# Performance work log

Measured on AMD Instinct MI355X. Metric: run time of the kernel, lower is better.

Reference implementation:

```python
import jax
jax.config.update("jax_enable_x64", True)
import jax.numpy as jnp
import numpy as np

B, T, C, H = 4, 4096, 120, 64  # batch, seq, n_embed, head_size


def setup_inputs() -> dict:
    key = jax.random.key(0)
    kx, kk, kq, kv = jax.random.split(key, 4)
    x = jax.random.normal(kx, (B, T, C), dtype=jnp.float32)
    s = 1.0 / np.sqrt(C)  # ~nn.Linear init scale
    Wk = jax.random.normal(kk, (C, H), dtype=jnp.float32) * s
    Wq = jax.random.normal(kq, (C, H), dtype=jnp.float32) * s
    Wv = jax.random.normal(kv, (C, H), dtype=jnp.float32) * s
    return {"x": x, "Wk": Wk, "Wq": Wq, "Wv": Wv}


def reference(x, Wk, Wq, Wv):
    # Original module runs entirely in float64 (.double()).
    x = x.astype(jnp.float64)
    Wk = Wk.astype(jnp.float64)
    Wq = Wq.astype(jnp.float64)
    Wv = Wv.astype(jnp.float64)
    k = jnp.einsum("btc,ch->bth", x, Wk)
    q = jnp.einsum("btc,ch->bth", x, Wq)
    v = jnp.einsum("btc,ch->bth", x, Wv)
    scale = x.shape[-1] ** (-0.5)  # NOTE: scales by n_embed (C), not head_size
    wei = jnp.einsum("bth,bsh->bts", q, k) * scale  # [B, T, T]
    wei = jax.nn.softmax(wei, axis=-1)
    # dropout(p=0.01) is identity in eval mode
    out = jnp.einsum("bts,bsh->bth", wei, v)  # [B, T, H]
    return out
```

## Files before the change

### kernel.cpp

```cpp
#include <hip/hip_runtime.h>

typedef __attribute__((ext_vector_type(2))) float f32x2;
typedef __attribute__((ext_vector_type(4))) float f32x4;
typedef __attribute__((ext_vector_type(8))) short s16x8;
typedef __attribute__((ext_vector_type(2))) unsigned int u32x2;
typedef __attribute__((ext_vector_type(4))) unsigned int u32x4;

#define BN 4
#define TN 4096
#define CN 120
#define HN 64

__device__ __forceinline__ unsigned short f2bf(float f) {
  unsigned int u = __float_as_uint(f);
  unsigned int r = (u + 0x7fffu + ((u >> 16) & 1u)) >> 16;
  return (unsigned short)r;
}
__device__ __forceinline__ float fast_exp2(float x) {
#if __has_builtin(__builtin_amdgcn_exp2f)
  return __builtin_amdgcn_exp2f(x);
#else
  return exp2f(x);
#endif
}


__global__ __launch_bounds__(256, 2) void proj_kernel(
    const float* __restrict__ x, const float* __restrict__ Wk,
    const float* __restrict__ Wq, const float* __restrict__ Wv,
    unsigned short* __restrict__ Kf, unsigned short* __restrict__ Qg,
    unsigned short* __restrict__ Vf) {
  __shared__ struct {
    float w[CN][HN];
    union {
      float xr[64][124];
      unsigned short vt[64][72];
    } u;
  } sm;
  const int tid = threadIdx.x;
  const int mat = blockIdx.x >> 8;
  const int rb = blockIdx.x & 255;
  const int row0 = rb * 64;
  const float* Ws = (mat == 0) ? Wk : (mat == 1) ? Wq : Wv;
  {
    const f32x4* s = (const f32x4*)Ws;
    f32x4* d = (f32x4*)&sm.w[0][0];
    for (int i = tid; i < CN * HN / 4; i += 256) d[i] = s[i];
  }
  for (int n = tid; n < 64 * 30; n += 256) {
    const int row = n / 30, c4 = n - row * 30;
    *(f32x4*)&sm.u.xr[row][c4 * 4] =
        *(const f32x4*)&x[(size_t)(row0 + row) * CN + c4 * 4];
  }
  __syncthreads();
  const int hg = tid & 15;
  const int rg = tid >> 4;
  f32x4 acc[4];
#pragma unroll
  for (int r = 0; r < 4; ++r) acc[r] = 0.f;
  for (int c = 0; c < CN; c += 4) {
    f32x4 xv[4];
#pragma unroll
    for (int r = 0; r < 4; ++r) xv[r] = *(const f32x4*)&sm.u.xr[rg * 4 + r][c];
#pragma unroll
    for (int cc = 0; cc < 4; ++cc) {
      const f32x4 wv = *(const f32x4*)&sm.w[c + cc][hg * 4];
#pragma unroll
      for (int r = 0; r < 4; ++r) acc[r] += wv * xv[r][cc];
    }
  }
  const int b = row0 >> 12, key0 = row0 & (TN - 1);
  if (mat == 1) {
    const float sc = 0.13169944f;
#pragma unroll
    for (int r = 0; r < 4; ++r) {
      u32x2 wd;
      wd.x = (unsigned int)f2bf(acc[r][0] * sc) |
             ((unsigned int)f2bf(acc[r][1] * sc) << 16);
      wd.y = (unsigned int)f2bf(acc[r][2] * sc) |
             ((unsigned int)f2bf(acc[r][3] * sc) << 16);
      *(u32x2*)&Qg[(size_t)(row0 + rg * 4 + r) * HN + hg * 4] = wd;
    }
  } else if (mat == 0) {
    __syncthreads();
#pragma unroll
    for (int r = 0; r < 4; ++r) {
      u32x2 wd;
      wd.x = (unsigned int)f2bf(acc[r][0]) |
             ((unsigned int)f2bf(acc[r][1]) << 16);
      wd.y = (unsigned int)f2bf(acc[r][2]) |
             ((unsigned int)f2bf(acc[r][3]) << 16);
      *(u32x2*)&sm.u.vt[rg * 4 + r][hg * 4] = wd;
    }
    __syncthreads();
#pragma unroll
    for (int i = 0; i < 2; ++i) {
      const int c = tid + i * 256;
      const int ktl = c >> 7, ch = (c >> 6) & 1, L = c & 63;
      const u32x4 d =
          *(const u32x4*)&sm.u.vt[ktl * 16 + (L & 15)][(L >> 4) * 8 + ch * 32];
      *(u32x4*)((unsigned char*)Kf +
                (((size_t)b * 256 + (key0 >> 4) + ktl) * 128 + ch * 64 + L) *
                    16) = d;
    }
  } else {
    __syncthreads();
#pragma unroll
    for (int r = 0; r < 4; ++r)
#pragma unroll
      for (int j = 0; j < 4; ++j)
        sm.u.vt[hg * 4 + j][rg * 4 + r] = f2bf(acc[r][j]);
    __syncthreads();
#pragma unroll
    for (int i = 0; i < 2; ++i) {
      const int c = tid + i * 256;
      const int kbl = c >> 8, ht = (c >> 6) & 3, L = c & 63;
      const u32x4 d =
          *(const u32x4*)&sm.u.vt[ht * 16 + (L & 15)][kbl * 32 + (L >> 4) * 8];
      *(u32x4*)((unsigned char*)Vf +
                (((size_t)b * 128 + (key0 >> 5) + kbl) * 4 + ht) * 1024 +
                L * 16) = d;
    }
  }
}

__global__ __launch_bounds__(512, 4) void attn_kernel(
    const unsigned short* __restrict__ Qg, const unsigned short* __restrict__ Kf,
    const unsigned short* __restrict__ Vf, float* __restrict__ out) {
  __shared__ union {
    unsigned short p[8][2][16][72];
    struct { float ob[8][64][17]; float lb[8][16]; } m;
  } sm;
  const int bid = blockIdx.x;
  const int xslot = bid & 7;
  const int b = xslot >> 1;
  const int qt5 = (bid >> 3) | ((xslot & 1) << 6);
  const int qbase = qt5 * 32;
  const int tid = threadIdx.x;
  const int wave = tid >> 6, lane = tid & 63;
  const int l15 = lane & 15, quad = lane >> 4;

  s16x8 qf[2][2];
#pragma unroll
  for (int qt = 0; qt < 2; ++qt) {
    const unsigned short* qrow =
        Qg + (size_t)(b * TN + qbase + qt * 16 + l15) * HN + quad * 8;
    qf[qt][0] = *(const s16x8*)qrow;
    qf[qt][1] = *(const s16x8*)(qrow + 32);
  }

  const unsigned char* Kfb = (const unsigned char*)Kf + (size_t)b * 524288;
  const unsigned char* Vfb = (const unsigned char*)Vf + (size_t)b * 524288;
  char* pw[2];
#pragma unroll
  for (int qt = 0; qt < 2; ++qt)
    pw[qt] = (char*)&sm.p[wave][qt][0][0] + l15 * 144;

  f32x4 o[2][4];
#pragma unroll
  for (int qt = 0; qt < 2; ++qt)
#pragma unroll
    for (int t = 0; t < 4; ++t) o[qt][t] = 0.f;
  float lacc[2] = {0.f, 0.f};

  const int kb0 = wave * 512;
#pragma unroll 1
  for (int it = 0; it < 8; ++it) {
    const int kb = kb0 + it * 64;
#pragma unroll
    for (int t = 0; t < 4; ++t) {
      const unsigned char* ktp =
          Kfb + (size_t)((kb >> 4) + t) * 2048 + lane * 16;
      const s16x8 a0 = *(const s16x8*)ktp;
      const s16x8 a1 = *(const s16x8*)(ktp + 1024);
      f32x4 s0 = 0.f, s1 = 0.f;
      s0 = __builtin_amdgcn_mfma_f32_16x16x32_bf16(a0, qf[0][0], s0, 0, 0, 0);
      s0 = __builtin_amdgcn_mfma_f32_16x16x32_bf16(a1, qf[0][1], s0, 0, 0, 0);
      s1 = __builtin_amdgcn_mfma_f32_16x16x32_bf16(a0, qf[1][0], s1, 0, 0, 0);
      s1 = __builtin_amdgcn_mfma_f32_16x16x32_bf16(a1, qf[1][1], s1, 0, 0, 0);
#pragma unroll
      for (int qt = 0; qt < 2; ++qt) {
        const f32x4 s = qt ? s1 : s0;
        unsigned int u0 = __float_as_uint(fast_exp2(fminf(s[0], 80.f)));
        unsigned int u1 = __float_as_uint(fast_exp2(fminf(s[1], 80.f)));
        unsigned int u2 = __float_as_uint(fast_exp2(fminf(s[2], 80.f)));
        unsigned int u3 = __float_as_uint(fast_exp2(fminf(s[3], 80.f)));
        u0 &= 0xffff0000u; u1 &= 0xffff0000u;
        u2 &= 0xffff0000u; u3 &= 0xffff0000u;
        lacc[qt] += (__uint_as_float(u0) + __uint_as_float(u1)) +
                    (__uint_as_float(u2) + __uint_as_float(u3));
        u32x2 w;
        w.x = (u0 >> 16) | u1;
        w.y = (u2 >> 16) | u3;
        *(u32x2*)(pw[qt] + t * 32 + quad * 8) = w;
      }
    }
#pragma unroll 1
    for (int kc = 0; kc < 2; ++kc) {
      const s16x8 pb0 = *(const s16x8*)(pw[0] + quad * 16 + kc * 64);
      const s16x8 pb1 = *(const s16x8*)(pw[1] + quad * 16 + kc * 64);
#pragma unroll
      for (int ht = 0; ht < 4; ++ht) {
        const unsigned char* vtp =
            Vfb + (size_t)((kb >> 5) + kc) * 4096 + ht * 1024 + lane * 16;
        const s16x8 va = *(const s16x8*)vtp;
        o[0][ht] = __builtin_amdgcn_mfma_f32_16x16x32_bf16(va, pb0, o[0][ht], 0, 0, 0);
        o[1][ht] = __builtin_amdgcn_mfma_f32_16x16x32_bf16(va, pb1, o[1][ht], 0, 0, 0);
      }
    }
  }
#pragma unroll
  for (int qt = 0; qt < 2; ++qt) {
    lacc[qt] += __shfl_xor(lacc[qt], 16, 64);
    lacc[qt] += __shfl_xor(lacc[qt], 32, 64);
  }
  __syncthreads();
#pragma unroll
  for (int qt = 0; qt < 2; ++qt) {
    if (lane < 16) sm.m.lb[wave][l15] = lacc[qt];
#pragma unroll
    for (int ht = 0; ht < 4; ++ht)
#pragma unroll
      for (int r = 0; r < 4; ++r)
        sm.m.ob[wave][ht * 16 + quad * 4 + r][l15] = o[qt][ht][r];
    __syncthreads();
    const int h = tid & 63;
    const int wq = tid >> 6;
#pragma unroll
    for (int i = 0; i < 2; ++i) {
      const int qq = (i << 3) | wq;
      float ssum = 0.f, ll = 0.f;
#pragma unroll
      for (int w = 0; w < 8; ++w) {
        ssum += sm.m.ob[w][h][qq];
        ll += sm.m.lb[w][qq];
      }
      out[(size_t)(b * TN + qbase + qt * 16 + qq) * HN + h] = ssum / ll;
    }
    __syncthreads();
  }
}

extern "C" void kernel_launch(void* const* d_in, const int* in_sizes, int n_in,
                              void* d_out, int out_size, void* d_ws,
                              size_t ws_size, hipStream_t stream) {
  const float* x = (const float*)d_in[0];
  const float* Wk = (const float*)d_in[1];
  const float* Wq = (const float*)d_in[2];
  const float* Wv = (const float*)d_in[3];
  unsigned short* Kf = (unsigned short*)d_ws;
  unsigned short* Qg = Kf + (size_t)BN * TN * HN;
  unsigned short* Vf = Qg + (size_t)BN * TN * HN;
  float* out = (float*)d_out;
  proj_kernel<<<768, 256, 0, stream>>>(x, Wk, Wq, Wv, Kf, Qg, Vf);
  attn_kernel<<<BN * TN / 32, 512, 0, stream>>>(Qg, Kf, Vf, out);
}
```

Measured before the change: 114.3 us.

## Process 64 query rows per attention block to reuse K/V fragments

```diff
diff --git a/kernel.cpp b/kernel.cpp
--- a/kernel.cpp
+++ b/kernel.cpp
@@ -124,25 +124,25 @@
   }
 }
 
-__global__ __launch_bounds__(512, 4) void attn_kernel(
+__global__ __launch_bounds__(512, 2) void attn_kernel(
     const unsigned short* __restrict__ Qg, const unsigned short* __restrict__ Kf,
     const unsigned short* __restrict__ Vf, float* __restrict__ out) {
   __shared__ union {
-    unsigned short p[8][2][16][72];
+    unsigned short p[8][4][16][40];
     struct { float ob[8][64][17]; float lb[8][16]; } m;
   } sm;
   const int bid = blockIdx.x;
   const int xslot = bid & 7;
   const int b = xslot >> 1;
-  const int qt5 = (bid >> 3) | ((xslot & 1) << 6);
-  const int qbase = qt5 * 32;
+  const int qr = (bid >> 3) | ((xslot & 1) << 5);
+  const int qbase = qr * 64;
   const int tid = threadIdx.x;
   const int wave = tid >> 6, lane = tid & 63;
   const int l15 = lane & 15, quad = lane >> 4;
 
-  s16x8 qf[2][2];
-#pragma unroll
-  for (int qt = 0; qt < 2; ++qt) {
+  s16x8 qf[4][2];
+#pragma unroll
+  for (int qt = 0; qt < 4; ++qt) {
     const unsigned short* qrow =
         Qg + (size_t)(b * TN + qbase + qt * 16 + l15) * HN + quad * 8;
     qf[qt][0] = *(const s16x8*)qrow;
@@ -151,72 +151,80 @@
 
   const unsigned char* Kfb = (const unsigned char*)Kf + (size_t)b * 524288;
   const unsigned char* Vfb = (const unsigned char*)Vf + (size_t)b * 524288;
-  char* pw[2];
-#pragma unroll
-  for (int qt = 0; qt < 2; ++qt)
-    pw[qt] = (char*)&sm.p[wave][qt][0][0] + l15 * 144;
-
-  f32x4 o[2][4];
-#pragma unroll
-  for (int qt = 0; qt < 2; ++qt)
+  char* pw[4];
+#pragma unroll
+  for (int qt = 0; qt < 4; ++qt)
+    pw[qt] = (char*)&sm.p[wave][qt][0][0] + l15 * 80;
+
+  f32x4 o[4][4];
+#pragma unroll
+  for (int qt = 0; qt < 4; ++qt)
 #pragma unroll
     for (int t = 0; t < 4; ++t) o[qt][t] = 0.f;
-  float lacc[2] = {0.f, 0.f};
+  float lacc[4] = {0.f, 0.f, 0.f, 0.f};
 
   const int kb0 = wave * 512;
 #pragma unroll 1
   for (int it = 0; it < 8; ++it) {
     const int kb = kb0 + it * 64;
 #pragma unroll
-    for (int t = 0; t < 4; ++t) {
-      const unsigned char* ktp =
-          Kfb + (size_t)((kb >> 4) + t) * 2048 + lane * 16;
-      const s16x8 a0 = *(const s16x8*)ktp;
-      const s16x8 a1 = *(const s16x8*)(ktp + 1024);
-      f32x4 s0 = 0.f, s1 = 0.f;
-      s0 = __builtin_amdgcn_mfma_f32_16x16x32_bf16(a0, qf[0][0], s0, 0, 0, 0);
-      s0 = __builtin_amdgcn_mfma_f32_16x16x32_bf16(a1, qf[0][1], s0, 0, 0, 0);
-      s1 = __builtin_amdgcn_mfma_f32_16x16x32_bf16(a0, qf[1][0], s1, 0, 0, 0);
-      s1 = __builtin_amdgcn_mfma_f32_16x16x32_bf16(a1, qf[1][1], s1, 0, 0, 0);
-#pragma unroll
-      for (int qt = 0; qt < 2; ++qt) {
-        const f32x4 s = qt ? s1 : s0;
-        unsigned int u0 = __float_as_uint(fast_exp2(fminf(s[0], 80.f)));
-        unsigned int u1 = __float_as_uint(fast_exp2(fminf(s[1], 80.f)));
-        unsigned int u2 = __float_as_uint(fast_exp2(fminf(s[2], 80.f)));
-        unsigned int u3 = __float_as_uint(fast_exp2(fminf(s[3], 80.f)));
-        u0 &= 0xffff0000u; u1 &= 0xffff0000u;
-        u2 &= 0xffff0000u; u3 &= 0xffff0000u;
-        lacc[qt] += (__uint_as_float(u0) + __uint_as_float(u1)) +
-                    (__uint_as_float(u2) + __uint_as_float(u3));
-        u32x2 w;
-        w.x = (u0 >> 16) | u1;
-        w.y = (u2 >> 16) | u3;
-        *(u32x2*)(pw[qt] + t * 32 + quad * 8) = w;
+    for (int half = 0; half < 2; ++half) {
+#pragma unroll
+      for (int t2 = 0; t2 < 2; ++t2) {
+        const unsigned char* ktp =
+            Kfb + (size_t)((kb >> 4) + half * 2 + t2) * 2048 + lane * 16;
+        const s16x8 a0 = *(const s16x8*)ktp;
+        const s16x8 a1 = *(const s16x8*)(ktp + 1024);
+        f32x4 s0 = 0.f, s1 = 0.f, s2 = 0.f, s3 = 0.f;
+        s0 = __builtin_amdgcn_mfma_f32_16x16x32_bf16(a0, qf[0][0], s0, 0, 0, 0);
+        s0 = __builtin_amdgcn_mfma_f32_16x16x32_bf16(a1, qf[0][1], s0, 0, 0, 0);
+        s1 = __builtin_amdgcn_mfma_f32_16x16x32_bf16(a0, qf[1][0], s1, 0, 0, 0);
+        s1 = __builtin_amdgcn_mfma_f32_16x16x32_bf16(a1, qf[1][1], s1, 0, 0, 0);
+        s2 = __builtin_amdgcn_mfma_f32_16x16x32_bf16(a0, qf[2][0], s2, 0, 0, 0);
+        s2 = __builtin_amdgcn_mfma_f32_16x16x32_bf16(a1, qf[2][1], s2, 0, 0, 0);
+        s3 = __builtin_amdgcn_mfma_f32_16x16x32_bf16(a0, qf[3][0], s3, 0, 0, 0);
+        s3 = __builtin_amdgcn_mfma_f32_16x16x32_bf16(a1, qf[3][1], s3, 0, 0, 0);
+#pragma unroll
+        for (int qt = 0; qt < 4; ++qt) {
+          const f32x4 s = (qt == 0) ? s0 : (qt == 1) ? s1 : (qt == 2) ? s2 : s3;
+          unsigned int u0 = __float_as_uint(fast_exp2(fminf(s[0], 80.f)));
+          unsigned int u1 = __float_as_uint(fast_exp2(fminf(s[1], 80.f)));
+          unsigned int u2 = __float_as_uint(fast_exp2(fminf(s[2], 80.f)));
+          unsigned int u3 = __float_as_uint(fast_exp2(fminf(s[3], 80.f)));
+          u0 &= 0xffff0000u; u1 &= 0xffff0000u;
+          u2 &= 0xffff0000u; u3 &= 0xffff0000u;
+          lacc[qt] += (__uint_as_float(u0) + __uint_as_float(u1)) +
+                      (__uint_as_float(u2) + __uint_as_float(u3));
+          u32x2 w;
+          w.x = (u0 >> 16) | u1;
+          w.y = (u2 >> 16) | u3;
+          *(u32x2*)(pw[qt] + t2 * 32 + quad * 8) = w;
+        }
       }
-    }
-#pragma unroll 1
-    for (int kc = 0; kc < 2; ++kc) {
-      const s16x8 pb0 = *(const s16x8*)(pw[0] + quad * 16 + kc * 64);
-      const s16x8 pb1 = *(const s16x8*)(pw[1] + quad * 16 + kc * 64);
+      const s16x8 pb0 = *(const s16x8*)(pw[0] + quad * 16);
+      const s16x8 pb1 = *(const s16x8*)(pw[1] + quad * 16);
+      const s16x8 pb2 = *(const s16x8*)(pw[2] + quad * 16);
+      const s16x8 pb3 = *(const s16x8*)(pw[3] + quad * 16);
 #pragma unroll
       for (int ht = 0; ht < 4; ++ht) {
         const unsigned char* vtp =
-            Vfb + (size_t)((kb >> 5) + kc) * 4096 + ht * 1024 + lane * 16;
+            Vfb + (size_t)((kb >> 5) + half) * 4096 + ht * 1024 + lane * 16;
         const s16x8 va = *(const s16x8*)vtp;
         o[0][ht] = __builtin_amdgcn_mfma_f32_16x16x32_bf16(va, pb0, o[0][ht], 0, 0, 0);
         o[1][ht] = __builtin_amdgcn_mfma_f32_16x16x32_bf16(va, pb1, o[1][ht], 0, 0, 0);
+        o[2][ht] = __builtin_amdgcn_mfma_f32_16x16x32_bf16(va, pb2, o[2][ht], 0, 0, 0);
+        o[3][ht] = __builtin_amdgcn_mfma_f32_16x16x32_bf16(va, pb3, o[3][ht], 0, 0, 0);
       }
     }
   }
 #pragma unroll
-  for (int qt = 0; qt < 2; ++qt) {
+  for (int qt = 0; qt < 4; ++qt) {
     lacc[qt] += __shfl_xor(lacc[qt], 16, 64);
     lacc[qt] += __shfl_xor(lacc[qt], 32, 64);
   }
   __syncthreads();
 #pragma unroll
-  for (int qt = 0; qt < 2; ++qt) {
+  for (int qt = 0; qt < 4; ++qt) {
     if (lane < 16) sm.m.lb[wave][l15] = lacc[qt];
 #pragma unroll
     for (int ht = 0; ht < 4; ++ht)
@@ -253,5 +261,5 @@
   unsigned short* Vf = Qg + (size_t)BN * TN * HN;
   float* out = (float*)d_out;
   proj_kernel<<<768, 256, 0, stream>>>(x, Wk, Wq, Wv, Kf, Qg, Vf);
-  attn_kernel<<<BN * TN / 32, 512, 0, stream>>>(Qg, Kf, Vf, out);
-}
+  attn_kernel<<<256, 512, 0, stream>>>(Qg, Kf, Vf, out);
+}
```

New measurement: 126.7 us. 10.8% more time.

## Compute QKV projection with split-bf16 MFMA instead of fp32 FMA

Applied to the files above, without the earlier changes.

```diff
diff --git a/kernel.cpp b/kernel.cpp
--- a/kernel.cpp
+++ b/kernel.cpp
@@ -15,6 +15,9 @@
   unsigned int u = __float_as_uint(f);
   unsigned int r = (u + 0x7fffu + ((u >> 16) & 1u)) >> 16;
   return (unsigned short)r;
+}
+__device__ __forceinline__ float bf2f(unsigned short h) {
+  return __uint_as_float((unsigned int)h << 16);
 }
 __device__ __forceinline__ float fast_exp2(float x) {
 #if __has_builtin(__builtin_amdgcn_exp2f)
@@ -25,98 +28,115 @@
 }
 
 
-__global__ __launch_bounds__(256, 2) void proj_kernel(
+__global__ __launch_bounds__(256, 3) void proj_kernel(
     const float* __restrict__ x, const float* __restrict__ Wk,
     const float* __restrict__ Wq, const float* __restrict__ Wv,
     unsigned short* __restrict__ Kf, unsigned short* __restrict__ Qg,
     unsigned short* __restrict__ Vf) {
   __shared__ struct {
-    float w[CN][HN];
-    union {
-      float xr[64][124];
-      unsigned short vt[64][72];
-    } u;
+    unsigned short xh[64][136];
+    unsigned short xl[64][136];
+    unsigned short vt[64][72];
   } sm;
   const int tid = threadIdx.x;
   const int mat = blockIdx.x >> 8;
   const int rb = blockIdx.x & 255;
   const int row0 = rb * 64;
+  const int wave = tid >> 6, lane = tid & 63;
+  const int l15 = lane & 15, quad = lane >> 4;
+  const int b = row0 >> 12, key0 = row0 & (TN - 1);
+
   const float* Ws = (mat == 0) ? Wk : (mat == 1) ? Wq : Wv;
-  {
-    const f32x4* s = (const f32x4*)Ws;
-    f32x4* d = (f32x4*)&sm.w[0][0];
-    for (int i = tid; i < CN * HN / 4; i += 256) d[i] = s[i];
-  }
+  const float wsc = (mat == 1) ? 0.13169944f : 1.0f;
+  s16x8 wh[4], wl[4];
+#pragma unroll
+  for (int kc = 0; kc < 4; ++kc) {
+#pragma unroll
+    for (int j = 0; j < 8; ++j) {
+      const int c = kc * 32 + quad * 8 + j;
+      const float w = (c < CN) ? Ws[c * HN + wave * 16 + l15] * wsc : 0.f;
+      const unsigned short h16 = f2bf(w);
+      wh[kc][j] = (short)h16;
+      wl[kc][j] = (short)f2bf(w - bf2f(h16));
+    }
+  }
+
   for (int n = tid; n < 64 * 30; n += 256) {
     const int row = n / 30, c4 = n - row * 30;
-    *(f32x4*)&sm.u.xr[row][c4 * 4] =
-        *(const f32x4*)&x[(size_t)(row0 + row) * CN + c4 * 4];
+    const f32x4 xv = *(const f32x4*)&x[(size_t)(row0 + row) * CN + c4 * 4];
+    u32x2 hp, lp;
+#pragma unroll
+    for (int e = 0; e < 2; ++e) {
+      const unsigned short h0 = f2bf(xv[2 * e]);
+      const unsigned short h1 = f2bf(xv[2 * e + 1]);
+      hp[e] = (unsigned int)h0 | ((unsigned int)h1 << 16);
+      lp[e] = (unsigned int)f2bf(xv[2 * e] - bf2f(h0)) |
+              ((unsigned int)f2bf(xv[2 * e + 1] - bf2f(h1)) << 16);
+    }
+    *(u32x2*)&sm.xh[row][c4 * 4] = hp;
+    *(u32x2*)&sm.xl[row][c4 * 4] = lp;
+  }
+  if (tid < 64) {
+    const u32x4 z = {0u, 0u, 0u, 0u};
+    *(u32x4*)&sm.xh[tid][120] = z;
+    *(u32x4*)&sm.xl[tid][120] = z;
   }
   __syncthreads();
-  const int hg = tid & 15;
-  const int rg = tid >> 4;
+
   f32x4 acc[4];
 #pragma unroll
-  for (int r = 0; r < 4; ++r) acc[r] = 0.f;
-  for (int c = 0; c < CN; c += 4) {
-    f32x4 xv[4];
-#pragma unroll
-    for (int r = 0; r < 4; ++r) xv[r] = *(const f32x4*)&sm.u.xr[rg * 4 + r][c];
-#pragma unroll
-    for (int cc = 0; cc < 4; ++cc) {
-      const f32x4 wv = *(const f32x4*)&sm.w[c + cc][hg * 4];
-#pragma unroll
-      for (int r = 0; r < 4; ++r) acc[r] += wv * xv[r][cc];
-    }
-  }
-  const int b = row0 >> 12, key0 = row0 & (TN - 1);
-  if (mat == 1) {
-    const float sc = 0.13169944f;
-#pragma unroll
-    for (int r = 0; r < 4; ++r) {
-      u32x2 wd;
-      wd.x = (unsigned int)f2bf(acc[r][0] * sc) |
-             ((unsigned int)f2bf(acc[r][1] * sc) << 16);
-      wd.y = (unsigned int)f2bf(acc[r][2] * sc) |
-             ((unsigned int)f2bf(acc[r][3] * sc) << 16);
-      *(u32x2*)&Qg[(size_t)(row0 + rg * 4 + r) * HN + hg * 4] = wd;
-    }
-  } else if (mat == 0) {
-    __syncthreads();
-#pragma unroll
-    for (int r = 0; r < 4; ++r) {
-      u32x2 wd;
-      wd.x = (unsigned int)f2bf(acc[r][0]) |
-             ((unsigned int)f2bf(acc[r][1]) << 16);
-      wd.y = (unsigned int)f2bf(acc[r][2]) |
-             ((unsigned int)f2bf(acc[r][3]) << 16);
-      *(u32x2*)&sm.u.vt[rg * 4 + r][hg * 4] = wd;
-    }
-    __syncthreads();
-#pragma unroll
-    for (int i = 0; i < 2; ++i) {
-      const int c = tid + i * 256;
-      const int ktl = c >> 7, ch = (c >> 6) & 1, L = c & 63;
-      const u32x4 d =
-          *(const u32x4*)&sm.u.vt[ktl * 16 + (L & 15)][(L >> 4) * 8 + ch * 32];
-      *(u32x4*)((unsigned char*)Kf +
-                (((size_t)b * 256 + (key0 >> 4) + ktl) * 128 + ch * 64 + L) *
-                    16) = d;
+  for (int mt = 0; mt < 4; ++mt) acc[mt] = 0.f;
+#pragma unroll
+  for (int mt = 0; mt < 4; ++mt) {
+#pragma unroll
+    for (int kc = 0; kc < 4; ++kc) {
+      const s16x8 ah = *(const s16x8*)&sm.xh[mt * 16 + l15][kc * 32 + quad * 8];
+      const s16x8 al = *(const s16x8*)&sm.xl[mt * 16 + l15][kc * 32 + quad * 8];
+      acc[mt] = __builtin_amdgcn_mfma_f32_16x16x32_bf16(al, wh[kc], acc[mt], 0, 0, 0);
+      acc[mt] = __builtin_amdgcn_mfma_f32_16x16x32_bf16(ah, wl[kc], acc[mt], 0, 0, 0);
+      acc[mt] = __builtin_amdgcn_mfma_f32_16x16x32_bf16(ah, wh[kc], acc[mt], 0, 0, 0);
+    }
+  }
+
+  if (mat < 2) {
+#pragma unroll
+    for (int mt = 0; mt < 4; ++mt)
+#pragma unroll
+      for (int r = 0; r < 4; ++r)
+        sm.vt[mt * 16 + quad * 4 + r][wave * 16 + l15] = f2bf(acc[mt][r]);
+    __syncthreads();
+    if (mat == 1) {
+      const int row = tid >> 2, seg = tid & 3;
+      const u32x4 d0 = *(const u32x4*)&sm.vt[row][seg * 16];
+      const u32x4 d1 = *(const u32x4*)&sm.vt[row][seg * 16 + 8];
+      unsigned short* qp = &Qg[(size_t)(row0 + row) * HN + seg * 16];
+      *(u32x4*)qp = d0;
+      *(u32x4*)(qp + 8) = d1;
+    } else {
+#pragma unroll
+      for (int i = 0; i < 2; ++i) {
+        const int c = tid + i * 256;
+        const int ktl = c >> 7, ch = (c >> 6) & 1, L = c & 63;
+        const u32x4 d =
+            *(const u32x4*)&sm.vt[ktl * 16 + (L & 15)][(L >> 4) * 8 + ch * 32];
+        *(u32x4*)((unsigned char*)Kf +
+                  (((size_t)b * 256 + (key0 >> 4) + ktl) * 128 + ch * 64 + L) *
+                      16) = d;
+      }
     }
   } else {
-    __syncthreads();
-#pragma unroll
-    for (int r = 0; r < 4; ++r)
-#pragma unroll
-      for (int j = 0; j < 4; ++j)
-        sm.u.vt[hg * 4 + j][rg * 4 + r] = f2bf(acc[r][j]);
+#pragma unroll
+    for (int mt = 0; mt < 4; ++mt)
+#pragma unroll
+      for (int r = 0; r < 4; ++r)
+        sm.vt[wave * 16 + l15][mt * 16 + quad * 4 + r] = f2bf(acc[mt][r]);
     __syncthreads();
 #pragma unroll
     for (int i = 0; i < 2; ++i) {
       const int c = tid + i * 256;
       const int kbl = c >> 8, ht = (c >> 6) & 3, L = c & 63;
       const u32x4 d =
-          *(const u32x4*)&sm.u.vt[ht * 16 + (L & 15)][kbl * 32 + (L >> 4) * 8];
+          *(const u32x4*)&sm.vt[ht * 16 + (L & 15)][kbl * 32 + (L >> 4) * 8];
       *(u32x4*)((unsigned char*)Vf +
                 (((size_t)b * 128 + (key0 >> 5) + kbl) * 4 + ht) * 1024 +
                 L * 16) = d;
```

Result: faster. 99.56 us (-12.9%).
